# Kernel optimization log

Measured on AMD Instinct MI355X. Metric: run time of the kernel, lower is better.

The kernel has to match this reference:

```python
import jax, jax.numpy as jnp
import numpy as np

N_HEAD, D_HEAD, D_MODEL = 8, 64, 512
MEM_LEN, QLEN, BSZ = 1024, 1024, 4
KLEN = MEM_LEN + QLEN
CONV_PAD = 3  # conv_size // 2 for conv_size = 7
LN_EPS = 1e-5


def setup_inputs() -> dict:
    key = jax.random.key(0)
    ks = jax.random.split(key, 16)
    s = 0.02
    inp = {
        "w": jax.random.normal(ks[0], (QLEN, BSZ, D_MODEL), jnp.float32),
        "r": jax.random.normal(ks[1], (KLEN, D_MODEL), jnp.float32),
        "mems": jax.random.normal(ks[2], (MEM_LEN, BSZ, D_MODEL), jnp.float32),
        "r_w_bias": jax.random.normal(ks[3], (N_HEAD, D_HEAD), jnp.float32) * s,
        "r_r_bias": jax.random.normal(ks[4], (N_HEAD, D_HEAD), jnp.float32) * s,
        "qkv_W": jax.random.normal(ks[5], (3 * N_HEAD * D_HEAD, D_MODEL), jnp.float32) * s,
        "r_W": jax.random.normal(ks[6], (N_HEAD * D_HEAD, D_MODEL), jnp.float32) * s,
        "conv_q_w": jax.random.normal(ks[7], (D_HEAD, D_HEAD, 7), jnp.float32) * 0.05,
        "conv_q_b": jnp.zeros((D_HEAD,), jnp.float32),
        "conv_k_w": jax.random.normal(ks[8], (D_HEAD, D_HEAD, 7), jnp.float32) * 0.05,
        "conv_k_b": jnp.zeros((D_HEAD,), jnp.float32),
        "conv_v_w": jax.random.normal(ks[9], (D_HEAD, D_HEAD, 7), jnp.float32) * 0.05,
        "conv_v_b": jnp.zeros((D_HEAD,), jnp.float32),
        "o_W": jax.random.normal(ks[10], (D_MODEL, N_HEAD * D_HEAD), jnp.float32) * s,
        "ln_g": jnp.ones((D_MODEL,), jnp.float32),
        "ln_b": jnp.zeros((D_MODEL,), jnp.float32),
        # causal-with-memory mask: query i may attend keys j <= i + MEM_LEN
        "attn_mask": jnp.arange(KLEN)[None, :] > (jnp.arange(QLEN)[:, None] + MEM_LEN),
    }
    return inp


def _conv1d(x, wt, b):
    # x: [N, C, L], wt: [O, I, K], same padding (pad=3)
    y = jax.lax.conv_general_dilated(x, wt, (1,), [(CONV_PAD, CONV_PAD)],
                                     dimension_numbers=("NCH", "OIH", "NCH"))
    return y + b[None, :, None]


def _head_conv(x, wt, b, length, bsz):
    # x: [len, b, H*Dh] -> per-head Conv1d over time -> [len, b, H, Dh]
    xh = x.reshape(length, bsz, N_HEAD, D_HEAD).transpose(2, 1, 3, 0)  # [H,b,Dh,len]
    xh = xh.reshape(N_HEAD * bsz, D_HEAD, length)
    xh = _conv1d(xh, wt, b)
    return xh.reshape(N_HEAD, bsz, D_HEAD, length).transpose(3, 1, 0, 2)  # [len,b,H,Dh]


def _rel_shift(x):
    # x: [qlen, rlen, b, n]
    q, rl, b, n = x.shape
    zp = jnp.zeros((q, 1, b, n), x.dtype)
    xp = jnp.concatenate([zp, x], axis=1).reshape(rl + 1, q, b, n)[1:]
    return xp.reshape(q, rl, b, n)


def _layer_norm(x, g, b):
    mu = jnp.mean(x, axis=-1, keepdims=True)
    var = jnp.mean(jnp.square(x - mu), axis=-1, keepdims=True)
    return (x - mu) * jax.lax.rsqrt(var + LN_EPS) * g + b


def reference(w, r, mems, r_w_bias, r_r_bias, qkv_W, r_W,
              conv_q_w, conv_q_b, conv_k_w, conv_k_b, conv_v_w, conv_v_b,
              o_W, ln_g, ln_b, attn_mask):
    qlen, bsz = w.shape[0], w.shape[1]
    cat = jnp.concatenate([mems, w], axis=0)           # [klen, b, d_model]
    klen = cat.shape[0]
    w_heads = cat @ qkv_W.T                            # [klen, b, 3*H*Dh]
    r_head_k = (r @ r_W.T).reshape(klen, N_HEAD, D_HEAD)
    q, k, v = jnp.split(w_heads, 3, axis=-1)
    q = q[-qlen:]
    # per-head conv augmentation of Q/K/V
    q = _head_conv(q, conv_q_w, conv_q_b, qlen, bsz)   # [qlen,b,H,Dh]
    k = _head_conv(k, conv_k_w, conv_k_b, klen, bsz)   # [klen,b,H,Dh]
    v = _head_conv(v, conv_v_w, conv_v_b, klen, bsz)
    scale = 1.0 / (D_HEAD ** 0.5)
    AC = jnp.einsum("ibnd,jbnd->ijbn", q + r_w_bias, k)
    BD = jnp.einsum("ibnd,jnd->ijbn", q + r_r_bias, r_head_k)
    BD = _rel_shift(BD)
    attn_score = (AC + BD) * scale                     # [qlen,klen,b,H]
    attn_score = jnp.where(attn_mask[:, :, None, None], -jnp.inf, attn_score)
    attn_prob = jax.nn.softmax(attn_score, axis=1)
    attn_vec = jnp.einsum("ijbn,jbnd->ibnd", attn_prob, v)
    attn_vec = attn_vec.reshape(qlen, bsz, N_HEAD * D_HEAD)
    attn_out = attn_vec @ o_W.T                        # [qlen,b,d_model]
    return _layer_norm(w + attn_out, ln_g, ln_b)
```

## Files before the change

kernel.cpp:

```cpp
#include <hip/hip_runtime.h>
#include <hip/hip_bf16.h>

typedef unsigned short u16;
typedef unsigned int   u32;
typedef u16 u16x8 __attribute__((ext_vector_type(8)));
typedef u16 u16x4 __attribute__((ext_vector_type(4)));
typedef float f32x4 __attribute__((ext_vector_type(4)));
typedef short s16x8 __attribute__((ext_vector_type(8)));
typedef u32 u32x4 __attribute__((ext_vector_type(4)));

__device__ __forceinline__ float b2f(u16 u) { return __uint_as_float(((u32)u) << 16); }
__device__ __forceinline__ u16 f2b(float f) {
  u32 u = __float_as_uint(f);
  u32 r = u + 0x7FFFu + ((u >> 16) & 1u);
  return (u16)(r >> 16);
}
__device__ __forceinline__ u32 f2b2(float lo, float hi) {
  __hip_bfloat162 h = __float22bfloat162_rn(make_float2(lo, hi));
  union { __hip_bfloat162 h; u32 u; } cv;
  cv.h = h;
  return cv.u;
}

#define MFMA_B16(A, B, C) __builtin_amdgcn_mfma_f32_16x16x32_bf16((A), (B), (C), 0, 0, 0)

__global__ __launch_bounds__(256) void cvt_all(
    const float* __restrict__ mems, const float* __restrict__ w,
    const float* __restrict__ r, const float* __restrict__ qkvW,
    const float* __restrict__ rW, const float* __restrict__ oW,
    u16* __restrict__ catb, u16* __restrict__ rb, u16* __restrict__ qkvWb,
    u16* __restrict__ rWb, u16* __restrict__ oWb) {
  long g = ((long)blockIdx.x * 256 + threadIdx.x) * 8;
  const float* src;
  u16* dst;
  if (g < 4194304) {
    src = (g < 2097152) ? (mems + g) : (w + (g - 2097152));
    dst = catb + g;
  } else if (g < 5242880) {
    src = r + (g - 4194304);    dst = rb + (g - 4194304);
  } else if (g < 6029312) {
    src = qkvW + (g - 5242880); dst = qkvWb + (g - 5242880);
  } else if (g < 6291456) {
    src = rW + (g - 6029312);   dst = rWb + (g - 6029312);
  } else {
    src = oW + (g - 6291456);   dst = oWb + (g - 6291456);
  }
  f32x4 a = *(const f32x4*)src;
  f32x4 b = *(const f32x4*)(src + 4);
  u32x4 p = (u32x4){f2b2(a[0], a[1]), f2b2(a[2], a[3]),
                    f2b2(b[0], b[1]), f2b2(b[2], b[3])};
  *(u32x4*)dst = p;
}

__global__ __launch_bounds__(256) void cvt_w(
    const float* __restrict__ cqw, const float* __restrict__ ckw,
    const float* __restrict__ cvw, u16* __restrict__ cwb) {
  int idx = blockIdx.x * 256 + threadIdx.x;
  if (idx >= 86016) return;
  int wsel = idx / 28672, rem = idx % 28672;
  const float* src = (wsel == 0) ? cqw : ((wsel == 1) ? ckw : cvw);
  int s = rem / 4096, r2 = rem % 4096;
  int d = r2 / 64, eswz = r2 % 64;
  int e = (((eswz >> 3) ^ (d & 7)) << 3) + (eswz & 7);
  cwb[idx] = f2b(src[d * 448 + e * 7 + s]);
}

__global__ __launch_bounds__(256) void gemm_fused(
    const u16* __restrict__ catb, const u16* __restrict__ qkvWb,
    u16* __restrict__ Wh, const u16* __restrict__ rb,
    const u16* __restrict__ rWb, u16* __restrict__ Rk) {
  int bx = blockIdx.x, by = blockIdx.y;
  const u16 *A, *B;
  u16* C;
  int N;
  if (bx < 12) {
    A = catb; B = qkvWb; C = Wh; N = 1536;
  } else {
    if (by >= 16) return;
    A = rb; B = rWb; C = Rk; N = 512; bx = 0;
  }
  const int K = 512;
  __shared__ u16 A_s[128 * 40];
  __shared__ u16 B_s[128 * 40];
  int tid = threadIdx.x;
  int wave = tid >> 6, lane = tid & 63, quad = lane >> 4, l16 = lane & 15;
  int wr = wave >> 1, wc = wave & 1;

  f32x4 acc[4][4];
#pragma unroll
  for (int a = 0; a < 4; a++)
#pragma unroll
    for (int bb = 0; bb < 4; bb++) acc[a][bb] = (f32x4){0.f, 0.f, 0.f, 0.f};

  int srow = tid >> 1;
  int kh = (tid & 1) * 16;
  const u16* ap = A + (size_t)(by * 128 + srow) * K + kh;
  const u16* bp = B + (size_t)(bx * 128 + srow) * K + kh;

  u16x8 pa0, pa1, pb0, pb1;
  pa0 = *(const u16x8*)(ap);
  pa1 = *(const u16x8*)(ap + 8);
  pb0 = *(const u16x8*)(bp);
  pb1 = *(const u16x8*)(bp + 8);

  for (int k0 = 0; k0 < K; k0 += 32) {
    __syncthreads();
    *(u16x8*)&A_s[srow * 40 + kh] = pa0;
    *(u16x8*)&A_s[srow * 40 + kh + 8] = pa1;
    *(u16x8*)&B_s[srow * 40 + kh] = pb0;
    *(u16x8*)&B_s[srow * 40 + kh + 8] = pb1;
    __syncthreads();

    int kn = k0 + 32;
    if (kn < K) {
      pa0 = *(const u16x8*)(ap + kn);
      pa1 = *(const u16x8*)(ap + kn + 8);
      pb0 = *(const u16x8*)(bp + kn);
      pb1 = *(const u16x8*)(bp + kn + 8);
    }

    s16x8 af[4], bf[4];
#pragma unroll
    for (int a = 0; a < 4; a++)
      af[a] = *(const s16x8*)&A_s[(wr * 64 + a * 16 + l16) * 40 + quad * 8];
#pragma unroll
    for (int bb = 0; bb < 4; bb++)
      bf[bb] = *(const s16x8*)&B_s[(wc * 64 + bb * 16 + l16) * 40 + quad * 8];
#pragma unroll
    for (int a = 0; a < 4; a++)
#pragma unroll
      for (int bb = 0; bb < 4; bb++)
        acc[a][bb] = MFMA_B16(af[a], bf[bb], acc[a][bb]);
  }

#pragma unroll
  for (int a = 0; a < 4; a++)
#pragma unroll
    for (int bb = 0; bb < 4; bb++) {
      int row = by * 128 + wr * 64 + a * 16 + quad * 4;
      int col = bx * 128 + wc * 64 + bb * 16 + l16;
#pragma unroll
      for (int reg = 0; reg < 4; reg++)
        C[(size_t)(row + reg) * N + col] = f2b(acc[a][bb][reg]);
    }
}

__global__ __launch_bounds__(256) void gemm_mfma(
    const u16* __restrict__ A, const u16* __restrict__ B,
    u16* __restrict__ C, int N, int K) {
  __shared__ u16 A_s[128 * 40];
  __shared__ u16 B_s[128 * 40];
  int tid = threadIdx.x;
  int bx = blockIdx.x, by = blockIdx.y;
  int wave = tid >> 6, lane = tid & 63, quad = lane >> 4, l16 = lane & 15;
  int wr = wave >> 1, wc = wave & 1;

  f32x4 acc[4][4];
#pragma unroll
  for (int a = 0; a < 4; a++)
#pragma unroll
    for (int bb = 0; bb < 4; bb++) acc[a][bb] = (f32x4){0.f, 0.f, 0.f, 0.f};

  int srow = tid >> 1;
  int kh = (tid & 1) * 16;
  const u16* ap = A + (size_t)(by * 128 + srow) * K + kh;
  const u16* bp = B + (size_t)(bx * 128 + srow) * K + kh;

  u16x8 pa0, pa1, pb0, pb1;
  pa0 = *(const u16x8*)(ap);
  pa1 = *(const u16x8*)(ap + 8);
  pb0 = *(const u16x8*)(bp);
  pb1 = *(const u16x8*)(bp + 8);

  for (int k0 = 0; k0 < K; k0 += 32) {
    __syncthreads();
    *(u16x8*)&A_s[srow * 40 + kh] = pa0;
    *(u16x8*)&A_s[srow * 40 + kh + 8] = pa1;
    *(u16x8*)&B_s[srow * 40 + kh] = pb0;
    *(u16x8*)&B_s[srow * 40 + kh + 8] = pb1;
    __syncthreads();

    int kn = k0 + 32;
    if (kn < K) {
      pa0 = *(const u16x8*)(ap + kn);
      pa1 = *(const u16x8*)(ap + kn + 8);
      pb0 = *(const u16x8*)(bp + kn);
      pb1 = *(const u16x8*)(bp + kn + 8);
    }

    s16x8 af[4], bf[4];
#pragma unroll
    for (int a = 0; a < 4; a++)
      af[a] = *(const s16x8*)&A_s[(wr * 64 + a * 16 + l16) * 40 + quad * 8];
#pragma unroll
    for (int bb = 0; bb < 4; bb++)
      bf[bb] = *(const s16x8*)&B_s[(wc * 64 + bb * 16 + l16) * 40 + quad * 8];
#pragma unroll
    for (int a = 0; a < 4; a++)
#pragma unroll
      for (int bb = 0; bb < 4; bb++)
        acc[a][bb] = MFMA_B16(af[a], bf[bb], acc[a][bb]);
  }

#pragma unroll
  for (int a = 0; a < 4; a++)
#pragma unroll
    for (int bb = 0; bb < 4; bb++) {
      int row = by * 128 + wr * 64 + a * 16 + quad * 4;
      int col = bx * 128 + wc * 64 + bb * 16 + l16;
#pragma unroll
      for (int reg = 0; reg < 4; reg++)
        C[(size_t)(row + reg) * N + col] = f2b(acc[a][bb][reg]);
    }
}

__global__ __launch_bounds__(256) void conv_fused(
    const u16* __restrict__ Wh, const u16* __restrict__ cwb,
    const float* __restrict__ cqb, const float* __restrict__ ckb,
    const float* __restrict__ cvb,
    u16* __restrict__ qpost, u16* __restrict__ kpost, u16* __restrict__ vpostT) {
  __shared__ u16 wT_s[7 * 4096];
  __shared__ u16 in_s[134 * 64];
  int tile = blockIdx.x;
  int part, t0, len, tshift, vt;
  const float* cbp;
  const u16* cwp;
  u16* outp;
  if (tile < 8) {
    part = 0; t0 = tile * 128; len = 1024; tshift = 1024; vt = 0;
    cbp = cqb; cwp = cwb; outp = qpost;
  } else if (tile < 24) {
    part = 1; t0 = (tile - 8) * 128; len = 2048; tshift = 0; vt = 0;
    cbp = ckb; cwp = cwb + 28672; outp = kpost;
  } else {
    part = 2; t0 = (tile - 24) * 128; len = 2048; tshift = 0; vt = 1;
    cbp = cvb; cwp = cwb + 57344; outp = vpostT;
  }
  int tid = threadIdx.x;
  int b = blockIdx.y, n = blockIdx.z;
  int wave = tid >> 6, lane = tid & 63, quad = lane >> 4, l16 = lane & 15;

  for (int idx = tid * 8; idx < 28672; idx += 2048)
    *(u16x8*)&wT_s[idx] = *(const u16x8*)(cwp + idx);
  {
    int e8 = tid & 7;
    int colb = part * 512 + n * 64 + e8 * 8;
    for (int r = tid >> 3; r < 134; r += 32) {
      int tt = t0 + r - 3;
      u16x8 v = {0, 0, 0, 0, 0, 0, 0, 0};
      if (tt >= 0 && tt < len)
        v = *(const u16x8*)(Wh + (size_t)((tt + tshift) * 4 + b) * 1536 + colb);
      *(u16x8*)&in_s[r * 64 + ((e8 ^ (r & 7)) << 3)] = v;
    }
  }
  __syncthreads();

  f32x4 acc[2][4];
#pragma unroll
  for (int mt = 0; mt < 2; mt++)
#pragma unroll
    for (int nn = 0; nn < 4; nn++) acc[mt][nn] = (f32x4){0.f, 0.f, 0.f, 0.f};

#pragma unroll
  for (int s = 0; s < 7; s++) {
#pragma unroll
    for (int ks = 0; ks < 2; ks++) {
      int eb = ks * 4 + quad;
      s16x8 af[2];
#pragma unroll
      for (int mt = 0; mt < 2; mt++) {
        int r = wave * 32 + mt * 16 + l16 + s;
        af[mt] = *(const s16x8*)&in_s[r * 64 + ((eb ^ (r & 7)) << 3)];
      }
#pragma unroll
      for (int nn = 0; nn < 4; nn++) {
        int d = nn * 16 + l16;
        s16x8 bf = *(const s16x8*)&wT_s[s * 4096 + d * 64 + ((eb ^ (d & 7)) << 3)];
        acc[0][nn] = MFMA_B16(af[0], bf, acc[0][nn]);
        acc[1][nn] = MFMA_B16(af[1], bf, acc[1][nn]);
      }
    }
  }

  float bias[4];
#pragma unroll
  for (int nn = 0; nn < 4; nn++) bias[nn] = cbp[nn * 16 + l16];

  if (!vt) {
#pragma unroll
    for (int mt = 0; mt < 2; mt++)
#pragma unroll
      for (int nn = 0; nn < 4; nn++) {
        int col = nn * 16 + l16;
#pragma unroll
        for (int reg = 0; reg < 4; reg++) {
          int t = t0 + wave * 32 + mt * 16 + quad * 4 + reg;
          outp[(size_t)((t * 4 + b) * 8 + n) * 64 + col] = f2b(acc[mt][nn][reg] + bias[nn]);
        }
      }
  } else {
    __syncthreads();
    u16* T = wT_s;
#pragma unroll
    for (int mt = 0; mt < 2; mt++)
#pragma unroll
      for (int nn = 0; nn < 4; nn++) {
        union { u32 u[2]; u16x4 v; } pk;
        pk.u[0] = f2b2(acc[mt][nn][0] + bias[nn], acc[mt][nn][1] + bias[nn]);
        pk.u[1] = f2b2(acc[mt][nn][2] + bias[nn], acc[mt][nn][3] + bias[nn]);
        *(u16x4*)&T[(nn * 16 + l16) * 136 + wave * 32 + mt * 16 + quad * 4] = pk.v;
      }
    __syncthreads();
    int dS = tid >> 2, tq = tid & 3;
    u16* gdst = outp + ((size_t)(b * 8 + n) * 64 + dS) * 2048 + t0 + tq * 32;
    const u16* tsrc = &T[dS * 136 + tq * 32];
#pragma unroll
    for (int c = 0; c < 4; c++)
      *(u16x8*)(gdst + c * 8) = *(const u16x8*)(tsrc + c * 8);
  }
}

__global__ __launch_bounds__(256) void attn_mfma(
    const u16* __restrict__ qpost, const u16* __restrict__ kpost,
    const u16* __restrict__ vpostT, const u16* __restrict__ Rk,
    const float* __restrict__ rwb, const float* __restrict__ rrb,
    u16* __restrict__ av_out) {
  __shared__ u16 K_s[64 * 64];
  __shared__ u16 V_s[64 * 64];
  __shared__ u16 R_s[128 * 64];
  __shared__ u16 BD_s[4][80 * 20];
  __shared__ u16 P_s[4][16 * 64];
  int tid = threadIdx.x;
  int bxr = blockIdx.x;
  int it = (bxr & 1) ? (15 - (bxr >> 1)) : (bxr >> 1);
  int i0 = it * 64, b = blockIdx.y, n = blockIdx.z;
  int wave = tid >> 6, lane = tid & 63, quad = lane >> 4, l16 = lane & 15;
  int i0w = i0 + wave * 16;
  int rbaseW = 48 - wave * 16;
  int rbase = 960 - i0;
  int ntiles = it + 17;
  const float SC = 0.125f * 1.44269504f;

  s16x8 aw[2], ar[2];
  {
    int ig = i0w + l16;
    const u16* qp = qpost + ((size_t)((ig * 4 + b) * 8 + n)) * 64;
#pragma unroll
    for (int ks = 0; ks < 2; ks++) {
      int d0 = ks * 32 + quad * 8;
      u16x8 qv = *(const u16x8*)(qp + d0);
      union { u32x4 u; s16x8 s; } pw, pr;
#pragma unroll
      for (int e2 = 0; e2 < 4; e2++) {
        float qa = b2f(qv[2 * e2]), qb = b2f(qv[2 * e2 + 1]);
        pw.u[e2] = f2b2(qa + rwb[n * 64 + d0 + 2 * e2], qb + rwb[n * 64 + d0 + 2 * e2 + 1]);
        pr.u[e2] = f2b2(qa + rrb[n * 64 + d0 + 2 * e2], qb + rrb[n * 64 + d0 + 2 * e2 + 1]);
      }
      aw[ks] = pw.s;
      ar[ks] = pr.s;
    }
  }

  {
    int rrI = tid >> 1, h = tid & 1;
    int g = rbase + rrI;
    int prow = g & 127;
    const u16* rp2 = Rk + (size_t)g * 512 + n * 64 + h * 32;
#pragma unroll
    for (int c = 0; c < 4; c++) {
      int kb = h * 4 + c;
      *(u16x8*)&R_s[prow * 64 + ((kb ^ (prow & 7)) << 3)] = *(const u16x8*)(rp2 + c * 8);
    }
  }

  f32x4 O[4];
#pragma unroll
  for (int c = 0; c < 4; c++) O[c] = (f32x4){0.f, 0.f, 0.f, 0.f};
  float l4[4] = {0.f, 0.f, 0.f, 0.f};

  int jl = tid >> 2, q4 = tid & 3;
  u16x8 kv0, kv1, vv0, vv1, rv0, rv1;
  {
    size_t src = ((size_t)(jl * 4 + b) * 8 + n) * 64 + q4 * 16;
    kv0 = *(const u16x8*)(kpost + src);
    kv1 = *(const u16x8*)(kpost + src + 8);
    const u16* vsrc = vpostT + ((size_t)(b * 8 + n) * 64 + jl) * 2048 + q4 * 16;
    vv0 = *(const u16x8*)(vsrc);
    vv1 = *(const u16x8*)(vsrc + 8);
  }
  {
    int g = rbase + 128 + jl;
    rv0 = (u16x8){0, 0, 0, 0, 0, 0, 0, 0};
    rv1 = rv0;
    if (g < 2048) {
      const u16* rp2 = Rk + (size_t)g * 512 + n * 64 + q4 * 16;
      rv0 = *(const u16x8*)(rp2);
      rv1 = *(const u16x8*)(rp2 + 8);
    }
  }

  for (int t = 0; t < ntiles; t++) {
    int j0 = t * 64;
    __syncthreads();
    *(u16x8*)&K_s[jl * 64 + (((2 * q4) ^ (jl & 7)) << 3)] = kv0;
    *(u16x8*)&K_s[jl * 64 + (((2 * q4 + 1) ^ (jl & 7)) << 3)] = kv1;
    *(u16x8*)&V_s[jl * 64 + (((2 * q4) ^ (jl & 7)) << 3)] = vv0;
    *(u16x8*)&V_s[jl * 64 + (((2 * q4 + 1) ^ (jl & 7)) << 3)] = vv1;
    if (t > 0) {
      int g = rbase + j0 + 64 + jl;
      int prow = g & 127;
      *(u16x8*)&R_s[prow * 64 + (((2 * q4) ^ (prow & 7)) << 3)] = rv0;
      *(u16x8*)&R_s[prow * 64 + (((2 * q4 + 1) ^ (prow & 7)) << 3)] = rv1;
    }
    __syncthreads();

    if (t + 1 < ntiles) {
      int j0n = j0 + 64;
      size_t src = ((size_t)((j0n + jl) * 4 + b) * 8 + n) * 64 + q4 * 16;
      kv0 = *(const u16x8*)(kpost + src);
      kv1 = *(const u16x8*)(kpost + src + 8);
      const u16* vsrc = vpostT + ((size_t)(b * 8 + n) * 64 + jl) * 2048 + j0n + q4 * 16;
      vv0 = *(const u16x8*)(vsrc);
      vv1 = *(const u16x8*)(vsrc + 8);
      int g = rbase + j0n + 64 + jl;
      rv0 = (u16x8){0, 0, 0, 0, 0, 0, 0, 0};
      rv1 = rv0;
      if (g < 2048) {
        const u16* rp2 = Rk + (size_t)g * 512 + n * 64 + q4 * 16;
        rv0 = *(const u16x8*)(rp2);
        rv1 = *(const u16x8*)(rp2 + 8);
      }
    }

    f32x4 sc4[4];
#pragma unroll
    for (int c = 0; c < 4; c++) {
      f32x4 tt = (f32x4){0.f, 0.f, 0.f, 0.f};
#pragma unroll
      for (int ks = 0; ks < 2; ks++) {
        int j = c * 16 + l16;
        int kb = ks * 4 + quad;
        s16x8 kf = *(const s16x8*)&K_s[j * 64 + ((kb ^ (j & 7)) << 3)];
        tt = MFMA_B16(aw[ks], kf, tt);
      }
      sc4[c] = tt;
    }
    int rbj = rbase + j0 + rbaseW;
#pragma unroll
    for (int cb = 0; cb < 5; cb++) {
      f32x4 tt = (f32x4){0.f, 0.f, 0.f, 0.f};
#pragma unroll
      for (int ks = 0; ks < 2; ks++) {
        int prow = (rbj + cb * 16 + l16) & 127;
        int kb = ks * 4 + quad;
        s16x8 rf = *(const s16x8*)&R_s[prow * 64 + ((kb ^ (prow & 7)) << 3)];
        tt = MFMA_B16(ar[ks], rf, tt);
      }
      union { u32 u[2]; u16x4 v; } pk;
      pk.u[0] = f2b2(tt[0], tt[1]);
      pk.u[1] = f2b2(tt[2], tt[3]);
      *(u16x4*)&BD_s[wave][(cb * 16 + l16) * 20 + quad * 4] = pk.v;
    }

#pragma unroll
    for (int c = 0; c < 4; c++)
#pragma unroll
      for (int reg = 0; reg < 4; reg++) {
        int iw = quad * 4 + reg;
        int uw = c * 16 + l16 + 15 - iw;
        float bd = b2f(BD_s[wave][uw * 20 + iw]);
        float val = (sc4[c][reg] + bd) * SC;
        int jg = j0 + c * 16 + l16;
        float p = (jg > i0w + iw + 1024) ? 0.f : __builtin_amdgcn_exp2f(val);
        l4[reg] += p;
        int jb = c * 2 + (l16 >> 3);
        P_s[wave][iw * 64 + ((jb ^ (iw & 7)) << 3) + (l16 & 7)] = f2b(p);
      }

#pragma unroll
    for (int cd = 0; cd < 4; cd++) {
      int d = cd * 16 + l16;
#pragma unroll
      for (int ks = 0; ks < 2; ks++) {
        int kb = ks * 4 + quad;
        s16x8 pf = *(const s16x8*)&P_s[wave][l16 * 64 + ((kb ^ (l16 & 7)) << 3)];
        s16x8 vf = *(const s16x8*)&V_s[d * 64 + ((kb ^ (d & 7)) << 3)];
        O[cd] = MFMA_B16(pf, vf, O[cd]);
      }
    }
  }

#pragma unroll
  for (int off = 1; off < 16; off <<= 1)
#pragma unroll
    for (int reg = 0; reg < 4; reg++) l4[reg] += __shfl_xor(l4[reg], off);

#pragma unroll
  for (int reg = 0; reg < 4; reg++) {
    float inv = 1.0f / l4[reg];
    int ig2 = i0w + quad * 4 + reg;
#pragma unroll
    for (int cd = 0; cd < 4; cd++)
      av_out[((size_t)(ig2 * 4 + b)) * 512 + n * 64 + cd * 16 + l16] =
          f2b(O[cd][reg] * inv);
  }
}

__global__ __launch_bounds__(64) void lnorm(
    const float* __restrict__ w, const u16* __restrict__ ao,
    const float* __restrict__ g, const float* __restrict__ bb,
    float* __restrict__ out) {
  int row = blockIdx.x, t = threadIdx.x;
  const float* wp = w + (size_t)row * 512 + t * 8;
  const u16* ap = ao + (size_t)row * 512 + t * 8;
  f32x4 w0 = *(const f32x4*)wp;
  f32x4 w1 = *(const f32x4*)(wp + 4);
  u16x8 av = *(const u16x8*)ap;
  float x[8];
  float sum = 0.f;
#pragma unroll
  for (int e = 0; e < 4; e++) {
    x[e] = w0[e] + b2f(av[e]);
    x[4 + e] = w1[e] + b2f(av[4 + e]);
  }
#pragma unroll
  for (int e = 0; e < 8; e++) sum += x[e];
#pragma unroll
  for (int off = 1; off < 64; off <<= 1) sum += __shfl_xor(sum, off);
  float mu = sum * (1.0f / 512.0f);
  float vs = 0.f;
#pragma unroll
  for (int e = 0; e < 8; e++) {
    float d = x[e] - mu;
    vs += d * d;
  }
#pragma unroll
  for (int off = 1; off < 64; off <<= 1) vs += __shfl_xor(vs, off);
  float rs = rsqrtf(vs * (1.0f / 512.0f) + 1e-5f);
  f32x4 g0 = *(const f32x4*)(g + t * 8);
  f32x4 g1 = *(const f32x4*)(g + t * 8 + 4);
  f32x4 b0 = *(const f32x4*)(bb + t * 8);
  f32x4 b1 = *(const f32x4*)(bb + t * 8 + 4);
  f32x4 o0, o1;
#pragma unroll
  for (int e = 0; e < 4; e++) {
    o0[e] = (x[e] - mu) * rs * g0[e] + b0[e];
    o1[e] = (x[4 + e] - mu) * rs * g1[e] + b1[e];
  }
  float* op = out + (size_t)row * 512 + t * 8;
  *(f32x4*)op = o0;
  *(f32x4*)(op + 4) = o1;
}

extern "C" void kernel_launch(void* const* d_in, const int* in_sizes, int n_in,
                              void* d_out, int out_size, void* d_ws, size_t ws_size,
                              hipStream_t stream) {
  (void)in_sizes; (void)n_in; (void)out_size;
  const float* w    = (const float*)d_in[0];
  const float* r    = (const float*)d_in[1];
  const float* mems = (const float*)d_in[2];
  const float* rwb  = (const float*)d_in[3];
  const float* rrb  = (const float*)d_in[4];
  const float* qkvW = (const float*)d_in[5];
  const float* rW   = (const float*)d_in[6];
  const float* cqw  = (const float*)d_in[7];
  const float* cqb  = (const float*)d_in[8];
  const float* ckw  = (const float*)d_in[9];
  const float* ckb  = (const float*)d_in[10];
  const float* cvw  = (const float*)d_in[11];
  const float* cvb  = (const float*)d_in[12];
  const float* oW   = (const float*)d_in[13];
  const float* lng  = (const float*)d_in[14];
  const float* lnb  = (const float*)d_in[15];

  u16* ws     = (u16*)d_ws;
  u16* Wh     = ws;
  u16* qpost  = Wh + 12582912;
  u16* kpost  = qpost + 2097152;
  u16* vpostT = kpost + 4194304;
  u16* Rk     = vpostT + 4194304;
  u16* av     = Rk + 1048576;
  u16* aout   = av + 2097152;
  u16* qkvWb  = aout + 2097152;
  u16* rWb    = qkvWb + 786432;
  u16* oWb    = rWb + 262144;
  u16* cwb    = oWb + 262144;
  u16* catb   = av;
  u16* rb     = qpost;
  if (ws_size < 59416576ull) return;

  cvt_all<<<3200, 256, 0, stream>>>(mems, w, r, qkvW, rW, oW, catb, rb, qkvWb, rWb, oWb);
  cvt_w<<<336, 256, 0, stream>>>(cqw, ckw, cvw, cwb);
  gemm_fused<<<dim3(13, 64), 256, 0, stream>>>(catb, qkvWb, Wh, rb, rWb, Rk);
  conv_fused<<<dim3(40, 4, 8), 256, 0, stream>>>(Wh, cwb, cqb, ckb, cvb, qpost, kpost, vpostT);
  attn_mfma<<<dim3(16, 4, 8), 256, 0, stream>>>(qpost, kpost, vpostT, Rk, rwb, rrb, av);
  gemm_mfma<<<dim3(4, 32), 256, 0, stream>>>(av, oWb, aout, 512, 512);
  lnorm<<<4096, 64, 0, stream>>>(w, aout, lng, lnb, (float*)d_out);
}
```

Measured before the change: 245.6 us.

## Split attention key range across two blocks and combine partial outputs

The attention kernel now splits each query tile's key loop into two halves handled by separate blocks, doubling the grid from 512 to 1024 blocks. Each half writes unnormalized fp32 partial outputs and row sums to workspace, and a new combine kernel adds them and normalizes to bf16. This is meant to improve occupancy and load balance on a GPU with many CUs. It costs an extra kernel launch and fp32 partial traffic. It also adds s_setprio around the MFMA sections. The combine is exact only because the softmax uses no running max, so the two halves share the same exponent scale.

```diff
diff --git a/kernel.cpp b/kernel.cpp
--- a/kernel.cpp
+++ b/kernel.cpp
@@ -324,7 +324,7 @@
     const u16* __restrict__ qpost, const u16* __restrict__ kpost,
     const u16* __restrict__ vpostT, const u16* __restrict__ Rk,
     const float* __restrict__ rwb, const float* __restrict__ rrb,
-    u16* __restrict__ av_out) {
+    float* __restrict__ Opart, float* __restrict__ lpart) {
   __shared__ u16 K_s[64 * 64];
   __shared__ u16 V_s[64 * 64];
   __shared__ u16 R_s[128 * 64];
@@ -332,13 +332,19 @@
   __shared__ u16 P_s[4][16 * 64];
   int tid = threadIdx.x;
   int bxr = blockIdx.x;
-  int it = (bxr & 1) ? (15 - (bxr >> 1)) : (bxr >> 1);
+  int half = bxr & 1;
+  int bq = bxr >> 1;
+  int it = (bq & 1) ? (15 - (bq >> 1)) : (bq >> 1);
   int i0 = it * 64, b = blockIdx.y, n = blockIdx.z;
   int wave = tid >> 6, lane = tid & 63, quad = lane >> 4, l16 = lane & 15;
   int i0w = i0 + wave * 16;
   int rbaseW = 48 - wave * 16;
   int rbase = 960 - i0;
-  int ntiles = it + 17;
+  int nt = it + 17;
+  int ht = (nt + 1) >> 1;
+  int t0h = half ? ht : 0;
+  int t1h = half ? nt : ht;
+  int j0s = t0h * 64;
   const float SC = 0.125f * 1.44269504f;
 
   s16x8 aw[2], ar[2];
@@ -363,7 +369,7 @@
 
   {
     int rrI = tid >> 1, h = tid & 1;
-    int g = rbase + rrI;
+    int g = rbase + j0s + rrI;
     int prow = g & 127;
     const u16* rp2 = Rk + (size_t)g * 512 + n * 64 + h * 32;
 #pragma unroll
@@ -381,15 +387,15 @@
   int jl = tid >> 2, q4 = tid & 3;
   u16x8 kv0, kv1, vv0, vv1, rv0, rv1;
   {
-    size_t src = ((size_t)(jl * 4 + b) * 8 + n) * 64 + q4 * 16;
+    size_t src = ((size_t)((j0s + jl) * 4 + b) * 8 + n) * 64 + q4 * 16;
     kv0 = *(const u16x8*)(kpost + src);
     kv1 = *(const u16x8*)(kpost + src + 8);
-    const u16* vsrc = vpostT + ((size_t)(b * 8 + n) * 64 + jl) * 2048 + q4 * 16;
+    const u16* vsrc = vpostT + ((size_t)(b * 8 + n) * 64 + jl) * 2048 + j0s + q4 * 16;
     vv0 = *(const u16x8*)(vsrc);
     vv1 = *(const u16x8*)(vsrc + 8);
   }
   {
-    int g = rbase + 128 + jl;
+    int g = rbase + j0s + 128 + jl;
     rv0 = (u16x8){0, 0, 0, 0, 0, 0, 0, 0};
     rv1 = rv0;
     if (g < 2048) {
@@ -399,14 +405,14 @@
     }
   }
 
-  for (int t = 0; t < ntiles; t++) {
+  for (int t = t0h; t < t1h; t++) {
     int j0 = t * 64;
     __syncthreads();
     *(u16x8*)&K_s[jl * 64 + (((2 * q4) ^ (jl & 7)) << 3)] = kv0;
     *(u16x8*)&K_s[jl * 64 + (((2 * q4 + 1) ^ (jl & 7)) << 3)] = kv1;
     *(u16x8*)&V_s[jl * 64 + (((2 * q4) ^ (jl & 7)) << 3)] = vv0;
     *(u16x8*)&V_s[jl * 64 + (((2 * q4 + 1) ^ (jl & 7)) << 3)] = vv1;
-    if (t > 0) {
+    if (t > t0h) {
       int g = rbase + j0 + 64 + jl;
       int prow = g & 127;
       *(u16x8*)&R_s[prow * 64 + (((2 * q4) ^ (prow & 7)) << 3)] = rv0;
@@ -414,7 +420,7 @@
     }
     __syncthreads();
 
-    if (t + 1 < ntiles) {
+    if (t + 1 < t1h) {
       int j0n = j0 + 64;
       size_t src = ((size_t)((j0n + jl) * 4 + b) * 8 + n) * 64 + q4 * 16;
       kv0 = *(const u16x8*)(kpost + src);
@@ -432,6 +438,7 @@
       }
     }
 
+    __builtin_amdgcn_s_setprio(1);
     f32x4 sc4[4];
 #pragma unroll
     for (int c = 0; c < 4; c++) {
@@ -461,6 +468,7 @@
       pk.u[1] = f2b2(tt[2], tt[3]);
       *(u16x4*)&BD_s[wave][(cb * 16 + l16) * 20 + quad * 4] = pk.v;
     }
+    __builtin_amdgcn_s_setprio(0);
 
 #pragma unroll
     for (int c = 0; c < 4; c++)
@@ -477,6 +485,7 @@
         P_s[wave][iw * 64 + ((jb ^ (iw & 7)) << 3) + (l16 & 7)] = f2b(p);
       }
 
+    __builtin_amdgcn_s_setprio(1);
 #pragma unroll
     for (int cd = 0; cd < 4; cd++) {
       int d = cd * 16 + l16;
@@ -488,6 +497,7 @@
         O[cd] = MFMA_B16(pf, vf, O[cd]);
       }
     }
+    __builtin_amdgcn_s_setprio(0);
   }
 
 #pragma unroll
@@ -495,15 +505,45 @@
 #pragma unroll
     for (int reg = 0; reg < 4; reg++) l4[reg] += __shfl_xor(l4[reg], off);
 
+  float* Ob = Opart + (size_t)half * 4096 * 512;
 #pragma unroll
   for (int reg = 0; reg < 4; reg++) {
-    float inv = 1.0f / l4[reg];
     int ig2 = i0w + quad * 4 + reg;
 #pragma unroll
     for (int cd = 0; cd < 4; cd++)
-      av_out[((size_t)(ig2 * 4 + b)) * 512 + n * 64 + cd * 16 + l16] =
-          f2b(O[cd][reg] * inv);
-  }
+      Ob[((size_t)(ig2 * 4 + b)) * 512 + n * 64 + cd * 16 + l16] = O[cd][reg];
+  }
+  if (l16 == 0) {
+#pragma unroll
+    for (int reg = 0; reg < 4; reg++) {
+      int ig2 = i0w + quad * 4 + reg;
+      lpart[half * 32768 + (ig2 * 4 + b) * 8 + n] = l4[reg];
+    }
+  }
+}
+
+__global__ __launch_bounds__(256) void attn_combine(
+    const float* __restrict__ Opart, const float* __restrict__ lpart,
+    u16* __restrict__ av) {
+  int idx = blockIdx.x * 256 + threadIdx.x;
+  int row = idx >> 6;
+  int c8 = (idx & 63) * 8;
+  int n = c8 >> 6;
+  const float* p0 = Opart + (size_t)row * 512 + c8;
+  const float* p1 = p0 + (size_t)4096 * 512;
+  float l = lpart[row * 8 + n] + lpart[32768 + row * 8 + n];
+  float inv = 1.f / l;
+  f32x4 a0 = *(const f32x4*)p0;
+  f32x4 a1 = *(const f32x4*)(p0 + 4);
+  f32x4 b0 = *(const f32x4*)p1;
+  f32x4 b1 = *(const f32x4*)(p1 + 4);
+  u16x8 o;
+#pragma unroll
+  for (int e = 0; e < 4; e++) {
+    o[e] = f2b((a0[e] + b0[e]) * inv);
+    o[4 + e] = f2b((a1[e] + b1[e]) * inv);
+  }
+  *(u16x8*)(av + (size_t)row * 512 + c8) = o;
 }
 
 __global__ __launch_bounds__(64) void lnorm(
@@ -587,13 +627,16 @@
   u16* cwb    = oWb + 262144;
   u16* catb   = av;
   u16* rb     = qpost;
+  float* Opart = (float*)d_ws;
+  float* lpart = (float*)d_ws + 4194304;
   if (ws_size < 59416576ull) return;
 
   cvt_all<<<3200, 256, 0, stream>>>(mems, w, r, qkvW, rW, oW, catb, rb, qkvWb, rWb, oWb);
   cvt_w<<<336, 256, 0, stream>>>(cqw, ckw, cvw, cwb);
   gemm_fused<<<dim3(13, 64), 256, 0, stream>>>(catb, qkvWb, Wh, rb, rWb, Rk);
   conv_fused<<<dim3(40, 4, 8), 256, 0, stream>>>(Wh, cwb, cqb, ckb, cvb, qpost, kpost, vpostT);
-  attn_mfma<<<dim3(16, 4, 8), 256, 0, stream>>>(qpost, kpost, vpostT, Rk, rwb, rrb, av);
+  attn_mfma<<<dim3(32, 4, 8), 256, 0, stream>>>(qpost, kpost, vpostT, Rk, rwb, rrb, Opart, lpart);
+  attn_combine<<<1024, 256, 0, stream>>>(Opart, lpart, av);
   gemm_mfma<<<dim3(4, 32), 256, 0, stream>>>(av, oWb, aout, 512, 512);
   lnorm<<<4096, 64, 0, stream>>>(w, aout, lng, lnb, (float*)d_out);
 }
```

Result: no change. 249.1 us (+1.4%).

## Load GEMM tiles directly into LDS and skip unused Q rows for memory part

Applied to the files above, without the earlier changes.

Both bf16 GEMM kernels now copy A/B tiles from global memory straight into LDS with global_load_lds, replacing the register-staged prefetch, and drop the padded LDS stride (40 to 32). The fused QKV GEMM also skips blocks that would compute Q projections for memory rows, which are discarded later. This removes register traffic and a VGPR round trip, but it loses the software prefetch overlap and may add LDS bank conflicts on the unpadded fragment reads.

```diff
diff --git a/kernel.cpp b/kernel.cpp
--- a/kernel.cpp
+++ b/kernel.cpp
@@ -23,6 +23,12 @@
 }
 
 #define MFMA_B16(A, B, C) __builtin_amdgcn_mfma_f32_16x16x32_bf16((A), (B), (C), 0, 0, 0)
+
+__device__ __forceinline__ void gl16(const u16* g, u16* l) {
+  __builtin_amdgcn_global_load_lds(
+      (const __attribute__((address_space(1))) void*)g,
+      (__attribute__((address_space(3))) void*)l, 16, 0, 0);
+}
 
 __global__ __launch_bounds__(256) void cvt_all(
     const float* __restrict__ mems, const float* __restrict__ w,
@@ -74,14 +80,15 @@
   u16* C;
   int N;
   if (bx < 12) {
+    if (bx < 4 && by < 32) return;
     A = catb; B = qkvWb; C = Wh; N = 1536;
   } else {
     if (by >= 16) return;
     A = rb; B = rWb; C = Rk; N = 512; bx = 0;
   }
   const int K = 512;
-  __shared__ u16 A_s[128 * 40];
-  __shared__ u16 B_s[128 * 40];
+  __shared__ u16 A_s[128 * 32];
+  __shared__ u16 B_s[128 * 32];
   int tid = threadIdx.x;
   int wave = tid >> 6, lane = tid & 63, quad = lane >> 4, l16 = lane & 15;
   int wr = wave >> 1, wc = wave & 1;
@@ -92,40 +99,30 @@
 #pragma unroll
     for (int bb = 0; bb < 4; bb++) acc[a][bb] = (f32x4){0.f, 0.f, 0.f, 0.f};
 
-  int srow = tid >> 1;
-  int kh = (tid & 1) * 16;
-  const u16* ap = A + (size_t)(by * 128 + srow) * K + kh;
-  const u16* bp = B + (size_t)(bx * 128 + srow) * K + kh;
-
-  u16x8 pa0, pa1, pb0, pb1;
-  pa0 = *(const u16x8*)(ap);
-  pa1 = *(const u16x8*)(ap + 8);
-  pb0 = *(const u16x8*)(bp);
-  pb1 = *(const u16x8*)(bp + 8);
+  const u16* Ab = A + (size_t)by * 128 * K;
+  const u16* Bb = B + (size_t)bx * 128 * K;
+  int lrow = lane >> 2;
+  int lkc  = (lane & 3) * 8;
+  int L0 = wave * 2;
 
   for (int k0 = 0; k0 < K; k0 += 32) {
     __syncthreads();
-    *(u16x8*)&A_s[srow * 40 + kh] = pa0;
-    *(u16x8*)&A_s[srow * 40 + kh + 8] = pa1;
-    *(u16x8*)&B_s[srow * 40 + kh] = pb0;
-    *(u16x8*)&B_s[srow * 40 + kh + 8] = pb1;
-    __syncthreads();
-
-    int kn = k0 + 32;
-    if (kn < K) {
-      pa0 = *(const u16x8*)(ap + kn);
-      pa1 = *(const u16x8*)(ap + kn + 8);
-      pb0 = *(const u16x8*)(bp + kn);
-      pb1 = *(const u16x8*)(bp + kn + 8);
-    }
+#pragma unroll
+    for (int m = 0; m < 2; m++) {
+      int L = L0 + m;
+      int row = L * 16 + lrow;
+      gl16(Ab + (size_t)row * K + k0 + lkc, &A_s[L * 512 + lane * 8]);
+      gl16(Bb + (size_t)row * K + k0 + lkc, &B_s[L * 512 + lane * 8]);
+    }
+    __syncthreads();
 
     s16x8 af[4], bf[4];
 #pragma unroll
     for (int a = 0; a < 4; a++)
-      af[a] = *(const s16x8*)&A_s[(wr * 64 + a * 16 + l16) * 40 + quad * 8];
+      af[a] = *(const s16x8*)&A_s[(wr * 64 + a * 16 + l16) * 32 + quad * 8];
 #pragma unroll
     for (int bb = 0; bb < 4; bb++)
-      bf[bb] = *(const s16x8*)&B_s[(wc * 64 + bb * 16 + l16) * 40 + quad * 8];
+      bf[bb] = *(const s16x8*)&B_s[(wc * 64 + bb * 16 + l16) * 32 + quad * 8];
 #pragma unroll
     for (int a = 0; a < 4; a++)
 #pragma unroll
@@ -148,8 +145,8 @@
 __global__ __launch_bounds__(256) void gemm_mfma(
     const u16* __restrict__ A, const u16* __restrict__ B,
     u16* __restrict__ C, int N, int K) {
-  __shared__ u16 A_s[128 * 40];
-  __shared__ u16 B_s[128 * 40];
+  __shared__ u16 A_s[128 * 32];
+  __shared__ u16 B_s[128 * 32];
   int tid = threadIdx.x;
   int bx = blockIdx.x, by = blockIdx.y;
   int wave = tid >> 6, lane = tid & 63, quad = lane >> 4, l16 = lane & 15;
@@ -161,40 +158,30 @@
 #pragma unroll
     for (int bb = 0; bb < 4; bb++) acc[a][bb] = (f32x4){0.f, 0.f, 0.f, 0.f};
 
-  int srow = tid >> 1;
-  int kh = (tid & 1) * 16;
-  const u16* ap = A + (size_t)(by * 128 + srow) * K + kh;
-  const u16* bp = B + (size_t)(bx * 128 + srow) * K + kh;
-
-  u16x8 pa0, pa1, pb0, pb1;
-  pa0 = *(const u16x8*)(ap);
-  pa1 = *(const u16x8*)(ap + 8);
-  pb0 = *(const u16x8*)(bp);
-  pb1 = *(const u16x8*)(bp + 8);
+  const u16* Ab = A + (size_t)by * 128 * K;
+  const u16* Bb = B + (size_t)bx * 128 * K;
+  int lrow = lane >> 2;
+  int lkc  = (lane & 3) * 8;
+  int L0 = wave * 2;
 
   for (int k0 = 0; k0 < K; k0 += 32) {
     __syncthreads();
-    *(u16x8*)&A_s[srow * 40 + kh] = pa0;
-    *(u16x8*)&A_s[srow * 40 + kh + 8] = pa1;
-    *(u16x8*)&B_s[srow * 40 + kh] = pb0;
-    *(u16x8*)&B_s[srow * 40 + kh + 8] = pb1;
-    __syncthreads();
-
-    int kn = k0 + 32;
-    if (kn < K) {
-      pa0 = *(const u16x8*)(ap + kn);
-      pa1 = *(const u16x8*)(ap + kn + 8);
-      pb0 = *(const u16x8*)(bp + kn);
-      pb1 = *(const u16x8*)(bp + kn + 8);
-    }
+#pragma unroll
+    for (int m = 0; m < 2; m++) {
+      int L = L0 + m;
+      int row = L * 16 + lrow;
+      gl16(Ab + (size_t)row * K + k0 + lkc, &A_s[L * 512 + lane * 8]);
+      gl16(Bb + (size_t)row * K + k0 + lkc, &B_s[L * 512 + lane * 8]);
+    }
+    __syncthreads();
 
     s16x8 af[4], bf[4];
 #pragma unroll
     for (int a = 0; a < 4; a++)
-      af[a] = *(const s16x8*)&A_s[(wr * 64 + a * 16 + l16) * 40 + quad * 8];
+      af[a] = *(const s16x8*)&A_s[(wr * 64 + a * 16 + l16) * 32 + quad * 8];
 #pragma unroll
     for (int bb = 0; bb < 4; bb++)
-      bf[bb] = *(const s16x8*)&B_s[(wc * 64 + bb * 16 + l16) * 40 + quad * 8];
+      bf[bb] = *(const s16x8*)&B_s[(wc * 64 + bb * 16 + l16) * 32 + quad * 8];
 #pragma unroll
     for (int a = 0; a < 4; a++)
 #pragma unroll
```

Result: faster. 239.3 us (-2.6%).
